# Optimization experiments

Measured on AMD Instinct MI355X. Metric: run time of the kernel, lower is better.

The kernel has to match this reference:

```python
import jax, jax.numpy as jnp
import numpy as np

H = 8          # heads
C = 128        # out_channels per head (hidden_dim)
EMB = 256      # embedding_dim
NG = 64        # number of graphs in batch
EPS_LN = 1e-5


def _layer_norm(x, g, b):
    mu = x.mean(-1, keepdims=True)
    var = ((x - mu) ** 2).mean(-1, keepdims=True)
    return (x - mu) * jax.lax.rsqrt(var + EPS_LN) * g + b


def _transformer_conv(x, src, dst, Wq, bq, Wk, bk, Wv, bv, Ws, bs, Wb):
    # PyG TransformerConv, heads=H, concat=False, beta=True, root_weight=True
    N = x.shape[0]
    q = (x @ Wq + bq).reshape(N, H, C)
    k = (x @ Wk + bk).reshape(N, H, C)
    v = (x @ Wv + bv).reshape(N, H, C)
    # per-edge attention logits: q_i . k_j / sqrt(C)   (i=dst, j=src)
    logits = jnp.einsum('ehc,ehc->eh', q[dst], k[src]) / jnp.sqrt(jnp.asarray(C, x.dtype))
    # segment softmax over incoming edges of each dst node
    m = jax.ops.segment_max(logits, dst, num_segments=N)
    m = jnp.where(jnp.isfinite(m), m, 0.0)
    ex = jnp.exp(logits - m[dst])
    den = jax.ops.segment_sum(ex, dst, num_segments=N)
    alpha = ex / (den[dst] + 1e-16)                      # [E,H]
    msg = alpha[:, :, None] * v[src]                     # [E,H,C]
    out = jax.ops.segment_sum(msg, dst, num_segments=N)  # [N,H,C]
    out = out.mean(axis=1)                               # concat=False -> head mean
    # beta-gated skip connection
    x_r = x @ Ws + bs                                    # [N,C]
    beta = jax.nn.sigmoid(jnp.concatenate([out, x_r, out - x_r], axis=-1) @ Wb)  # [N,1]
    return beta * x_r + (1.0 - beta) * out


def _lin(k, fan_in, fan_out, scale=None):
    s = scale if scale is not None else 1.0 / np.sqrt(fan_in)
    k1, k2 = jax.random.split(k)
    W = jax.random.uniform(k1, (fan_in, fan_out), jnp.float32, -s, s)
    b = jax.random.uniform(k2, (fan_out,), jnp.float32, -s, s)
    return W, b


def setup_inputs() -> dict:
    key = jax.random.key(0)
    ks = jax.random.split(key, 32)
    N, E, V = 50000, 400000, 10000
    inp = {
        'x': jax.random.randint(ks[0], (N,), 0, V, jnp.int32),
        'edge_index': jax.random.randint(ks[1], (2, E), 0, N, jnp.int32),
        'batch': jnp.sort(jax.random.randint(ks[2], (N,), 0, NG, jnp.int32)),
        'emb_w': jax.random.normal(ks[3], (V, EMB), jnp.float32),
    }
    ki = 4
    for l, din in enumerate([EMB, C]):
        Wq, bq = _lin(ks[ki], din, H * C); ki += 1
        Wk, bk = _lin(ks[ki], din, H * C); ki += 1
        Wv, bv = _lin(ks[ki], din, H * C); ki += 1
        Ws, bs = _lin(ks[ki], din, C); ki += 1
        Wb, _ = _lin(ks[ki], 3 * C, 1); ki += 1
        inp.update({f'Wq{l}': Wq, f'bq{l}': bq, f'Wk{l}': Wk, f'bk{l}': bk,
                    f'Wv{l}': Wv, f'bv{l}': bv, f'Ws{l}': Ws, f'bs{l}': bs,
                    f'Wb{l}': Wb, f'g{l}': jnp.ones((C,), jnp.float32),
                    f'be{l}': jnp.zeros((C,), jnp.float32)})
    Wc1, bc1 = _lin(ks[ki], C, C // 2); ki += 1
    Wc2, bc2 = _lin(ks[ki], C // 2, 1); ki += 1
    inp.update({'Wc1': Wc1, 'bc1': bc1, 'Wc2': Wc2, 'bc2': bc2})
    return inp


def reference(x, edge_index, batch, emb_w,
              Wq0, bq0, Wk0, bk0, Wv0, bv0, Ws0, bs0, Wb0, g0, be0,
              Wq1, bq1, Wk1, bk1, Wv1, bv1, Ws1, bs1, Wb1, g1, be1,
              Wc1, bc1, Wc2, bc2):
    src, dst = edge_index[0], edge_index[1]
    h = emb_w[x]                                           # [N, EMB]
    # layer 0 (no residual, per original `if i > 0`)
    h = _transformer_conv(h, src, dst, Wq0, bq0, Wk0, bk0, Wv0, bv0, Ws0, bs0, Wb0)
    h = jax.nn.relu(_layer_norm(h, g0, be0))               # dropout = identity (eval)
    # layer 1 (residual)
    res = h
    h = _transformer_conv(h, src, dst, Wq1, bq1, Wk1, bk1, Wv1, bv1, Ws1, bs1, Wb1)
    h = jax.nn.relu(_layer_norm(h + res, g1, be1))
    # global mean pool over graphs
    s = jax.ops.segment_sum(h, batch, num_segments=NG)     # [NG, C]
    cnt = jax.ops.segment_sum(jnp.ones((h.shape[0],), h.dtype), batch, num_segments=NG)
    pooled = s / jnp.maximum(cnt, 1.0)[:, None]
    # classifier MLP
    z = jax.nn.relu(pooled @ Wc1 + bc1)
    return z @ Wc2 + bc2                                   # [NG, 1]
```

## Files before the change

kernel.cpp:

```cpp
#include <hip/hip_runtime.h>
#include <hip/hip_fp16.h>
#include <math.h>

#define HEADS 8
#define CDIM 128
#define HC 1024
#define EMBD 256
#define NGRAPH 64
#define QSCALE2 0.12751744f

typedef unsigned short u16;
typedef short s8v __attribute__((ext_vector_type(8)));
typedef float f4v __attribute__((ext_vector_type(4)));
typedef _Float16 h2v __attribute__((ext_vector_type(2)));

__device__ __forceinline__ float b2f(u16 u) {
  union { unsigned int i; float f; } v; v.i = ((unsigned int)u) << 16; return v.f;
}
__device__ __forceinline__ u16 f2b(float f) {
  union { float f; unsigned int i; } v; v.f = f;
  unsigned int i = v.i;
  unsigned int r = (i + 0x7FFFu + ((i >> 16) & 1u)) >> 16;
  return (u16)r;
}
__device__ __forceinline__ u16 f2h(float f) {
  __half h = __float2half(f);
  return *(u16*)&h;
}

union U4H { uint4 u; h2v h[4]; };

__global__ __launch_bounds__(256) void embed_kernel(
    const int* __restrict__ x, const float* __restrict__ emb,
    u16* __restrict__ h0, int N)
{
  int idx = blockIdx.x * 256 + threadIdx.x;
  if (idx >= N * (EMBD / 4)) return;
  int n = idx >> 6;
  int j = (idx & 63) * 4;
  int vid = x[n];
  float4 f = *(const float4*)&emb[(size_t)vid * EMBD + j];
  ushort4 u;
  u.x = f2b(f.x); u.y = f2b(f.y); u.z = f2b(f.z); u.w = f2b(f.w);
  *(ushort4*)&h0[(size_t)n * EMBD + j] = u;
}

__global__ __launch_bounds__(256) void build_WsT_swz(
    const float* __restrict__ in, u16* __restrict__ out, int K)
{
  const int KS = K / 32;
  int nt = blockIdx.x;
  int ks = blockIdx.y;
  int t = threadIdx.x;
  int lane = t & 63, ni = t >> 6;
  int q4 = lane >> 4, cn = lane & 15;
  int colL = nt * 64 + ni * 16 + cn;
  int kbase = ks * 32 + q4 * 8;
  u16 tmp[8];
#pragma unroll
  for (int e8 = 0; e8 < 8; e8++) tmp[e8] = f2b(in[(size_t)(kbase + e8) * CDIM + colL]);
  size_t base = ((((size_t)nt * KS + ks) * 4 + ni) * 64 + lane) * 8;
  *(uint4*)&out[base] = *(uint4*)tmp;
}

__global__ __launch_bounds__(256) void build_qkvT_swz(
    const float* __restrict__ Wq, const float* __restrict__ Wk, const float* __restrict__ Wv,
    u16* __restrict__ WT, int K, int hpc)
{
  __shared__ u16 tile[64][130];
  const int KS = K / 32;
  int rg0 = blockIdx.x * 128;
  int kk0 = blockIdx.y * 64;
  int chunkCols = hpc * 384;
  int chunk = rg0 / chunkCols;
  int within = rg0 - chunk * chunkCols;
  int head = chunk * hpc + within / 384;
  int sub = within % 384;
  int sect = sub >> 7;
  const float* W = (sect == 0) ? Wq : (sect == 1 ? Wk : Wv);
  float scale = (sect == 0) ? QSCALE2 : 1.0f;
  int cc0 = head * CDIM;
  int t = threadIdx.x;
  int ci = t & 127, k2 = t >> 7;
#pragma unroll
  for (int ii = 0; ii < 32; ii++) {
    int ki = k2 + ii * 2;
    tile[ki][ci] = f2b(W[(size_t)(kk0 + ki) * HC + cc0 + ci] * scale);
  }
  __syncthreads();

  int lane = t & 63, ni = t >> 6;
  int q4 = lane >> 4, cn = lane & 15;
  int ntBase = rg0 >> 6;
#pragma unroll
  for (int ntd = 0; ntd < 2; ntd++) {
#pragma unroll
    for (int ksd = 0; ksd < 2; ksd++) {
      int colL = ntd * 64 + ni * 16 + cn;
      int kL = ksd * 32 + q4 * 8;
      u16 tmp[8];
#pragma unroll
      for (int e8 = 0; e8 < 8; e8++) tmp[e8] = tile[kL + e8][colL];
      size_t base = ((((size_t)(ntBase + ntd) * KS + (kk0 >> 5) + ksd) * 4 + ni) * 64 + lane) * 8;
      *(uint4*)&WT[base] = *(uint4*)tmp;
    }
  }
}
__global__ __launch_bounds__(256) void build_qkvb(
    const float* __restrict__ bq, const float* __restrict__ bk, const float* __restrict__ bv,
    float* __restrict__ bT, int hpc)
{
  int rg = blockIdx.x * 256 + threadIdx.x;
  if (rg >= 3 * HC) return;
  int chunkCols = hpc * 384;
  int chunk = rg / chunkCols;
  int within = rg - chunk * chunkCols;
  int head = chunk * hpc + within / 384;
  int sub = within % 384;
  int sect = sub >> 7;
  int cc = head * CDIM + (sub & 127);
  bT[rg] = (sect == 0) ? bq[cc] * QSCALE2 : (sect == 1 ? bk[cc] : bv[cc]);
}

__global__ __launch_bounds__(256) void deg_kernel(const int* __restrict__ ei, int* __restrict__ deg, int E) {
  int e = blockIdx.x * 256 + threadIdx.x;
  if (e < E) atomicAdd(&deg[ei[E + e]], 1);
}
__global__ __launch_bounds__(256) void scan1_kernel(const int* __restrict__ deg, int* __restrict__ row_ptr,
                                                    int* __restrict__ bsum, int N) {
  __shared__ int sb[256];
  int t = threadIdx.x, idx = blockIdx.x * 256 + t;
  int x = (idx < N) ? deg[idx] : 0;
  sb[t] = x; __syncthreads();
  for (int off = 1; off < 256; off <<= 1) {
    int y = (t >= off) ? sb[t - off] : 0;
    __syncthreads(); sb[t] += y; __syncthreads();
  }
  if (idx < N) row_ptr[idx + 1] = sb[t];
  if (t == 255) bsum[blockIdx.x] = sb[255];
  if (idx == 0) row_ptr[0] = 0;
}
__global__ __launch_bounds__(256) void scan2_kernel(int* __restrict__ bsum, int B) {
  __shared__ int sb[256];
  int t = threadIdx.x;
  int x = (t < B) ? bsum[t] : 0;
  sb[t] = x; __syncthreads();
  for (int off = 1; off < 256; off <<= 1) {
    int y = (t >= off) ? sb[t - off] : 0;
    __syncthreads(); sb[t] += y; __syncthreads();
  }
  if (t < B) bsum[t] = sb[t] - x;
}
__global__ __launch_bounds__(256) void scan3_kernel(int* __restrict__ row_ptr, const int* __restrict__ bsum, int N) {
  int idx = blockIdx.x * 256 + threadIdx.x;
  if (idx < N) row_ptr[idx + 1] += bsum[idx >> 8];
}
__global__ __launch_bounds__(256) void scatter_kernel(const int* __restrict__ ei,
                                                      const int* __restrict__ row_ptr,
                                                      int* __restrict__ fill, int* __restrict__ col, int E) {
  int e = blockIdx.x * 256 + threadIdx.x;
  if (e >= E) return;
  int d = ei[E + e];
  int pos = row_ptr[d] + atomicAdd(&fill[d], 1);
  col[pos] = ei[e];
}
__global__ void gb_kernel(const int* __restrict__ batch, int* __restrict__ gb, int N) {
  int g = threadIdx.x;
  if (g > NGRAPH) return;
  int lo = 0, hi = N;
  while (lo < hi) { int mid = (lo + hi) >> 1; if (batch[mid] < g) lo = mid + 1; else hi = mid; }
  gb[g] = lo;
}

template <int K>
__global__ __launch_bounds__(256, 3) void gemm_lds(
    const u16* __restrict__ A, const u16* __restrict__ Bq, const u16* __restrict__ Bx,
    int col0tile, int xrTile0,
    const float* __restrict__ biasQ, const float* __restrict__ biasX,
    u16* __restrict__ outQ, u16* __restrict__ outX,
    int M, int nTiles, int rowStrips, int nGroups)
{
  const int LDK = K + 8;
  const int KS = K / 32;
  __shared__ __align__(16) u16 As[64 * LDK];
  int B = blockIdx.x;
  int c8 = B & 7, kk = B >> 3;
  int tg = kk % nGroups;
  int s  = (kk / nGroups) * 8 + c8;
  if (s >= rowStrips) return;
  int t = threadIdx.x, lane = t & 63, w = t >> 6;
  int q4 = lane >> 4, cn = lane & 15;
  int m0 = s * 64;
  int ntL = tg * 4 + w;
  bool wActive = ntL < nTiles;
  int ntG = col0tile + ntL;
  bool isXr = ntG >= xrTile0;

  if (m0 + 64 <= M) {
    const u16* Ablk = A + (size_t)m0 * K;
#pragma unroll
    for (int ii = 0; ii < K / 32; ii++) {
      int g = (ii * 256 + t) * 8;
      int r = g / K, c = g - r * K;
      *(uint4*)&As[r * LDK + c] = *(const uint4*)(Ablk + g);
    }
  } else {
#pragma unroll
    for (int ii = 0; ii < K / 32; ii++) {
      int g = (ii * 256 + t) * 8;
      int r = g / K, c = g - r * K;
      int gr = m0 + r; if (gr >= M) gr = M - 1;
      *(uint4*)&As[r * LDK + c] = *(const uint4*)(A + (size_t)gr * K + c);
    }
  }
  __syncthreads();

  if (!wActive) return;

  f4v acc[4][4] = {};
  const u16* bb = isXr
      ? Bx + ((size_t)(ntG - xrTile0) * KS * 4) * 512 + lane * 8
      : Bq + ((size_t)ntG * KS * 4) * 512 + lane * 8;
#pragma unroll
  for (int ks = 0; ks < KS; ks++) {
    s8v bf[4], af[4];
#pragma unroll
    for (int ni = 0; ni < 4; ni++)
      bf[ni] = *(const s8v*)(bb + ((size_t)ks * 4 + ni) * 512);
#pragma unroll
    for (int mi = 0; mi < 4; mi++)
      af[mi] = *(const s8v*)&As[(mi * 16 + cn) * LDK + ks * 32 + q4 * 8];
#pragma unroll
    for (int mi = 0; mi < 4; mi++)
#pragma unroll
      for (int ni = 0; ni < 4; ni++)
        acc[mi][ni] = __builtin_amdgcn_mfma_f32_16x16x32_bf16(af[mi], bf[ni], acc[mi][ni], 0, 0, 0);
  }

  u16* obase = isXr ? outX + (size_t)(ntG - xrTile0) * M * 64
                    : outQ + (size_t)ntL * M * 64;
  float bv[4];
#pragma unroll
  for (int ni = 0; ni < 4; ni++)
    bv[ni] = isXr ? biasX[(ntG - xrTile0) * 64 + ni * 16 + cn]
                  : biasQ[ntG * 64 + ni * 16 + cn];
#pragma unroll
  for (int mi = 0; mi < 4; mi++) {
#pragma unroll
    for (int j = 0; j < 4; j++) {
      int gm = m0 + mi * 16 + q4 * 4 + j;
      if (gm < M) {
#pragma unroll
        for (int ni = 0; ni < 4; ni++) {
          float val = acc[mi][ni][j] + bv[ni];
          obase[(size_t)gm * 64 + ni * 16 + cn] = isXr ? f2b(val) : f2h(val);
        }
      }
    }
  }
}

template <int HPC>
__global__ __launch_bounds__(256) void attn_chunk_kernel(
    const u16* __restrict__ qkv,
    const int* __restrict__ row_ptr, const int* __restrict__ col,
    float* __restrict__ outacc, int N, int first)
{
  int t = threadIdx.x;
  int w = t >> 6, lane = t & 63;
  int g = lane >> 4, i = lane & 15;
  int n, j;
  if (HPC == 4)      { n = blockIdx.x;                 j = w; }
  else if (HPC == 2) { n = blockIdx.x * 2 + (w >> 1);  j = w & 1; }
  else               { n = blockIdx.x * 4 + w;         j = 0; }
  bool active = (HPC == 4) ? true : (n < N);

  int itile = i >> 3, ioff = (i & 7) * 8;
  const u16* qb = qkv + (size_t)(j * 6 + 0 + itile) * N * 64 + ioff;
  const u16* kb = qkv + (size_t)(j * 6 + 2 + itile) * N * 64 + ioff;
  const u16* vb = qkv + (size_t)(j * 6 + 4 + itile) * N * 64 + ioff;

  float acc[8] = {};
  float m = -INFINITY, l = 0.f;
  if (active) {
    U4H qu; qu.u = *(const uint4*)(qb + (size_t)n * 64);
    int e0 = row_ptr[n], e1 = row_ptr[n + 1];
    for (int eb = e0; eb < e1; eb += 8) {
      int egA = eb + g, egB = eb + 4 + g;
      bool vA = egA < e1, vB = egB < e1;
      int sA = col[vA ? egA : e1 - 1];
      int sB = col[vB ? egB : e1 - 1];
      U4H kuA, vuA, kuB, vuB;
      kuA.u = *(const uint4*)(kb + (size_t)sA * 64);
      kuB.u = *(const uint4*)(kb + (size_t)sB * 64);
      vuA.u = *(const uint4*)(vb + (size_t)sA * 64);
      vuB.u = *(const uint4*)(vb + (size_t)sB * 64);

      float pA, pB;
#if defined(__has_builtin) && __has_builtin(__builtin_amdgcn_fdot2)
      pA = __builtin_amdgcn_fdot2(kuA.h[0], qu.h[0], 0.f, false);
      pA = __builtin_amdgcn_fdot2(kuA.h[1], qu.h[1], pA, false);
      pA = __builtin_amdgcn_fdot2(kuA.h[2], qu.h[2], pA, false);
      pA = __builtin_amdgcn_fdot2(kuA.h[3], qu.h[3], pA, false);
      pB = __builtin_amdgcn_fdot2(kuB.h[0], qu.h[0], 0.f, false);
      pB = __builtin_amdgcn_fdot2(kuB.h[1], qu.h[1], pB, false);
      pB = __builtin_amdgcn_fdot2(kuB.h[2], qu.h[2], pB, false);
      pB = __builtin_amdgcn_fdot2(kuB.h[3], qu.h[3], pB, false);
#else
      pA = 0.f; pB = 0.f;
#pragma unroll
      for (int z = 0; z < 4; z++) {
        pA += (float)kuA.h[z][0] * (float)qu.h[z][0] + (float)kuA.h[z][1] * (float)qu.h[z][1];
        pB += (float)kuB.h[z][0] * (float)qu.h[z][0] + (float)kuB.h[z][1] * (float)qu.h[z][1];
      }
#endif
#pragma unroll
      for (int off = 1; off <= 8; off <<= 1) {
        pA += __shfl_xor(pA, off, 64);
        pB += __shfl_xor(pB, off, 64);
      }
      if (!vA) pA = -INFINITY;
      if (!vB) pB = -INFINITY;

      float pm = fmaxf(pA, pB);
      pm = fmaxf(pm, __shfl_xor(pm, 16));
      pm = fmaxf(pm, __shfl_xor(pm, 32));
      if (pm > m) {
        float al = exp2f(m - pm);
        l *= al;
#pragma unroll
        for (int z = 0; z < 8; z++) acc[z] *= al;
        m = pm;
      }
      float peA = exp2f(pA - m);
      float peB = exp2f(pB - m);
      float ps = peA + peB;
      ps += __shfl_xor(ps, 16);
      ps += __shfl_xor(ps, 32);
      l += ps;
#pragma unroll
      for (int z = 0; z < 4; z++) {
        acc[2 * z]     = fmaf(peA, (float)vuA.h[z][0], acc[2 * z]);
        acc[2 * z + 1] = fmaf(peA, (float)vuA.h[z][1], acc[2 * z + 1]);
      }
#pragma unroll
      for (int z = 0; z < 4; z++) {
        acc[2 * z]     = fmaf(peB, (float)vuB.h[z][0], acc[2 * z]);
        acc[2 * z + 1] = fmaf(peB, (float)vuB.h[z][1], acc[2 * z + 1]);
      }
    }
  }
  float inv = 0.125f / (l + 1e-16f);
#pragma unroll
  for (int z = 0; z < 8; z++) {
    float a = acc[z] * inv;
    a += __shfl_xor(a, 16);
    a += __shfl_xor(a, 32);
    acc[z] = a;
  }

  if (HPC == 1) {
    if (active && g == 0) {
      float* op = outacc + (size_t)n * CDIM + i * 8;
      if (first) {
        *(float4*)op       = make_float4(acc[0], acc[1], acc[2], acc[3]);
        *(float4*)(op + 4) = make_float4(acc[4], acc[5], acc[6], acc[7]);
      } else {
        float4 o0 = *(float4*)op, o1 = *(float4*)(op + 4);
        *(float4*)op       = make_float4(o0.x + acc[0], o0.y + acc[1], o0.z + acc[2], o0.w + acc[3]);
        *(float4*)(op + 4) = make_float4(o1.x + acc[4], o1.y + acc[5], o1.z + acc[6], o1.w + acc[7]);
      }
    }
  } else {
    __shared__ float sacc[4][128];
    if (g == 0) {
      *(float4*)&sacc[w][i * 8]     = make_float4(acc[0], acc[1], acc[2], acc[3]);
      *(float4*)&sacc[w][i * 8 + 4] = make_float4(acc[4], acc[5], acc[6], acc[7]);
    }
    __syncthreads();
    if (HPC == 4) {
      if (t < 128) {
        float v = sacc[0][t] + sacc[1][t] + sacc[2][t] + sacc[3][t];
        size_t o = (size_t)blockIdx.x * CDIM + t;
        outacc[o] = first ? v : (outacc[o] + v);
      }
    } else {
      int nn = blockIdx.x * 2 + (t >> 7);
      int c = t & 127;
      if (nn < N) {
        float v = sacc[(t >> 7) * 2][c] + sacc[(t >> 7) * 2 + 1][c];
        size_t o = (size_t)nn * CDIM + c;
        outacc[o] = first ? v : (outacc[o] + v);
      }
    }
  }
}

template <int LAYER>
__global__ __launch_bounds__(256) void epilogue_kernel(
    const float* __restrict__ outacc, const u16* __restrict__ xrT,
    const float* __restrict__ Wb, const float* __restrict__ gam, const float* __restrict__ bet,
    const u16* __restrict__ res,
    u16* __restrict__ hout, float* __restrict__ houtf, int N)
{
  int t = threadIdx.x;
  int local = t >> 7, c = t & 127, w = t >> 6;
  int n = blockIdx.x * 2 + local;
  bool act = n < N;
  __shared__ float sred[8];
  __shared__ float smv[2][3];

  float oc = 0.f, xc = 0.f;
  if (act) {
    oc = outacc[(size_t)n * CDIM + c];
    xc = b2f(xrT[((size_t)(c >> 6) * N + n) * 64 + (c & 63)]);
  }
  float pb = oc * Wb[c] + xc * Wb[CDIM + c] + (oc - xc) * Wb[2 * CDIM + c];
#pragma unroll
  for (int off = 32; off; off >>= 1) pb += __shfl_down(pb, off, 64);
  if ((t & 63) == 0) sred[w] = pb;
  __syncthreads();
  if (t == 0)   smv[0][0] = 1.f / (1.f + __expf(-(sred[0] + sred[1])));
  if (t == 128) smv[1][0] = 1.f / (1.f + __expf(-(sred[2] + sred[3])));
  __syncthreads();
  float beta = smv[local][0];
  float val = beta * xc + (1.f - beta) * oc;
  if (LAYER == 1 && act) val += b2f(res[(size_t)n * CDIM + c]);

  float s1 = val, s2 = val * val;
#pragma unroll
  for (int off = 32; off; off >>= 1) {
    s1 += __shfl_down(s1, off, 64);
    s2 += __shfl_down(s2, off, 64);
  }
  __syncthreads();
  if ((t & 63) == 0) { sred[w * 2] = s1; sred[w * 2 + 1] = s2; }
  __syncthreads();
  if (t == 0) {
    float S1 = sred[0] + sred[2], S2 = sred[1] + sred[3];
    float mu = S1 * (1.f / CDIM);
    float var = fmaxf(S2 * (1.f / CDIM) - mu * mu, 0.f);
    smv[0][1] = mu; smv[0][2] = 1.f / sqrtf(var + 1e-5f);
  }
  if (t == 128) {
    float S1 = sred[4] + sred[6], S2 = sred[5] + sred[7];
    float mu = S1 * (1.f / CDIM);
    float var = fmaxf(S2 * (1.f / CDIM) - mu * mu, 0.f);
    smv[1][1] = mu; smv[1][2] = 1.f / sqrtf(var + 1e-5f);
  }
  __syncthreads();
  if (act) {
    float y = (val - smv[local][1]) * smv[local][2] * gam[c] + bet[c];
    y = fmaxf(y, 0.f);
    if (LAYER == 0) hout[(size_t)n * CDIM + c] = f2b(y);
    else            houtf[(size_t)n * CDIM + c] = y;
  }
}

__global__ __launch_bounds__(256) void classifier_kernel(
    const float* __restrict__ hf, const int* __restrict__ gb,
    const float* __restrict__ Wc1, const float* __restrict__ bc1,
    const float* __restrict__ Wc2, const float* __restrict__ bc2,
    float* __restrict__ out)
{
  int g = blockIdx.x, t = threadIdx.x;
  int half = t >> 7, c = t & 127;
  int s = gb[g], e = gb[g + 1];
  float acc = 0.f;
  for (int n = s + half; n < e; n += 2) acc += hf[(size_t)n * CDIM + c];
  __shared__ float sb[2][128];
  __shared__ float sp[128], sz[64];
  sb[half][c] = acc;
  __syncthreads();
  float cg = fmaxf((float)(e - s), 1.f);
  if (t < 128) sp[t] = (sb[0][t] + sb[1][t]) / cg;
  __syncthreads();
  if (t < 64) {
    float a = bc1[t];
    for (int cc = 0; cc < 128; cc++) a += sp[cc] * Wc1[cc * 64 + t];
    sz[t] = fmaxf(a, 0.f);
  }
  __syncthreads();
  if (t < 64) {
    float pbv = sz[t] * Wc2[t];
    for (int off = 32; off; off >>= 1) pbv += __shfl_down(pbv, off, 64);
    if (t == 0) out[g] = pbv + bc2[0];
  }
}

extern "C" void kernel_launch(void* const* d_in, const int* in_sizes, int n_in,
                              void* d_out, int out_size, void* d_ws, size_t ws_size,
                              hipStream_t stream)
{
  if (n_in != 30) return;

  const int N = in_sizes[0];
  const int E = in_sizes[1] / 2;

  const int* x     = (const int*)d_in[0];
  const int* ei    = (const int*)d_in[1];
  const int* batch = (const int*)d_in[2];
  const float* emb = (const float*)d_in[3];
  const float* Wq0 = (const float*)d_in[4];  const float* bq0 = (const float*)d_in[5];
  const float* Wk0 = (const float*)d_in[6];  const float* bk0 = (const float*)d_in[7];
  const float* Wv0 = (const float*)d_in[8];  const float* bv0 = (const float*)d_in[9];
  const float* Ws0 = (const float*)d_in[10]; const float* bs0 = (const float*)d_in[11];
  const float* Wb0 = (const float*)d_in[12]; const float* g0  = (const float*)d_in[13]; const float* be0 = (const float*)d_in[14];
  const float* Wq1 = (const float*)d_in[15]; const float* bq1 = (const float*)d_in[16];
  const float* Wk1 = (const float*)d_in[17]; const float* bk1 = (const float*)d_in[18];
  const float* Wv1 = (const float*)d_in[19]; const float* bv1 = (const float*)d_in[20];
  const float* Ws1 = (const float*)d_in[21]; const float* bs1 = (const float*)d_in[22];
  const float* Wb1 = (const float*)d_in[23]; const float* g1  = (const float*)d_in[24]; const float* be1 = (const float*)d_in[25];
  const float* Wc1 = (const float*)d_in[26]; const float* bc1 = (const float*)d_in[27];
  const float* Wc2 = (const float*)d_in[28]; const float* bc2 = (const float*)d_in[29];

  auto rnd = [](size_t b) { return (b + 511) & ~(size_t)511; };
  size_t fixedBytes =
      rnd((size_t)N * CDIM * 4) +
      rnd((size_t)N * EMBD * 2) +
      rnd((size_t)N * CDIM * 2) * 2 +
      rnd((size_t)3 * HC * EMBD * 2) +
      rnd((size_t)3 * HC * CDIM * 2) +
      rnd((size_t)3 * HC * 4) * 2 +
      rnd((size_t)CDIM * EMBD * 2) +
      rnd((size_t)CDIM * CDIM * 2) +
      rnd((size_t)N * 4) * 2 +
      rnd((size_t)(N + 1) * 4) +
      rnd((size_t)E * 4) +
      rnd(256 * 4) +
      rnd(65 * 4);
  int hpc = 1;
  if (ws_size >= fixedBytes + rnd((size_t)N * 4 * 384 * 2)) hpc = 4;
  else if (ws_size >= fixedBytes + rnd((size_t)N * 2 * 384 * 2)) hpc = 2;
  const int chunkCols = hpc * 384;
  const int nchunks = HEADS / hpc;
  const int qkvTiles = chunkCols / 64;

  char* ws = (char*)d_ws;
  size_t off = 0;
  auto alloc = [&](size_t bytes) -> void* {
    void* p = ws + off;
    off += (bytes + 511) & ~(size_t)511;
    return p;
  };
  u16*   qkvc  = (u16*)  alloc((size_t)N * chunkCols * 2);
  float* outacc= (float*)alloc((size_t)N * CDIM * 4);
  u16*   h0    = (u16*)  alloc((size_t)N * EMBD * 2);
  u16*   h1    = (u16*)  alloc((size_t)N * CDIM * 2);
  u16*   xrb   = (u16*)  alloc((size_t)N * CDIM * 2);
  u16*   WT0   = (u16*)  alloc((size_t)3 * HC * EMBD * 2);
  u16*   WT1   = (u16*)  alloc((size_t)3 * HC * CDIM * 2);
  float* bT0   = (float*)alloc((size_t)3 * HC * 4);
  float* bT1   = (float*)alloc((size_t)3 * HC * 4);
  u16*   WsT0  = (u16*)  alloc((size_t)CDIM * EMBD * 2);
  u16*   WsT1  = (u16*)  alloc((size_t)CDIM * CDIM * 2);
  int*   deg   = (int*)  alloc((size_t)N * 4);
  int*   fill  = (int*)  alloc((size_t)N * 4);
  int*   rowp  = (int*)  alloc((size_t)(N + 1) * 4);
  int*   colb  = (int*)  alloc((size_t)E * 4);
  int*   bsum  = (int*)  alloc(256 * 4);
  int*   gb    = (int*)  alloc(65 * 4);

  hipMemsetAsync(deg, 0, (size_t)N * 4, stream);
  hipMemsetAsync(fill, 0, (size_t)N * 4, stream);

  embed_kernel<<<(N * 64 + 255) / 256, 256, 0, stream>>>(x, emb, h0, N);
  { dim3 gT(3 * HC / 128, EMBD / 64);
    build_qkvT_swz<<<gT, 256, 0, stream>>>(Wq0, Wk0, Wv0, WT0, EMBD, hpc); }
  { dim3 gT(3 * HC / 128, CDIM / 64);
    build_qkvT_swz<<<gT, 256, 0, stream>>>(Wq1, Wk1, Wv1, WT1, CDIM, hpc); }
  build_qkvb<<<(3 * HC + 255) / 256, 256, 0, stream>>>(bq0, bk0, bv0, bT0, hpc);
  build_qkvb<<<(3 * HC + 255) / 256, 256, 0, stream>>>(bq1, bk1, bv1, bT1, hpc);
  { dim3 gT(2, EMBD / 32);
    build_WsT_swz<<<gT, 256, 0, stream>>>(Ws0, WsT0, EMBD); }
  { dim3 gT(2, CDIM / 32);
    build_WsT_swz<<<gT, 256, 0, stream>>>(Ws1, WsT1, CDIM); }

  int nb = (N + 255) / 256;
  deg_kernel<<<(E + 255) / 256, 256, 0, stream>>>(ei, deg, E);
  scan1_kernel<<<nb, 256, 0, stream>>>(deg, rowp, bsum, N);
  scan2_kernel<<<1, 256, 0, stream>>>(bsum, nb);
  scan3_kernel<<<nb, 256, 0, stream>>>(rowp, bsum, N);
  scatter_kernel<<<(E + 255) / 256, 256, 0, stream>>>(ei, rowp, fill, colb, E);
  gb_kernel<<<1, 128, 0, stream>>>(batch, gb, N);

  int rowStrips = (N + 63) / 64;
  int sGroups = (rowStrips + 7) / 8;
  float* hfinal = (float*)h0;
  int epiBlocks = (N + 1) / 2;

  if (hpc == 4) {
    for (int layer = 0; layer < 2; layer++) {
      const u16* Ain   = (layer == 0) ? h0 : h1;
      const u16* WT    = (layer == 0) ? WT0 : WT1;
      const float* bT  = (layer == 0) ? bT0 : bT1;
      const u16* WsT   = (layer == 0) ? WsT0 : WsT1;
      const float* bs  = (layer == 0) ? bs0 : bs1;
      const float* Wb  = (layer == 0) ? Wb0 : Wb1;
      const float* gam = (layer == 0) ? g0 : g1;
      const float* bet = (layer == 0) ? be0 : be1;
      int K = (layer == 0) ? EMBD : CDIM;

      int nT0 = qkvTiles + 2;
      int nG0 = (nT0 + 3) / 4, nG1 = (qkvTiles + 3) / 4;
      int grid0 = sGroups * nG0 * 8, grid1 = sGroups * nG1 * 8;
      if (K == EMBD)
        gemm_lds<EMBD><<<grid0, 256, 0, stream>>>(Ain, WT, WsT, 0, qkvTiles, bT, bs, qkvc, xrb, N, nT0, rowStrips, nG0);
      else
        gemm_lds<CDIM><<<grid0, 256, 0, stream>>>(Ain, WT, WsT, 0, qkvTiles, bT, bs, qkvc, xrb, N, nT0, rowStrips, nG0);
      attn_chunk_kernel<4><<<N, 256, 0, stream>>>(qkvc, rowp, colb, outacc, N, 1);
      if (K == EMBD)
        gemm_lds<EMBD><<<grid1, 256, 0, stream>>>(Ain, WT, WsT, qkvTiles, 1 << 30, bT, bs, qkvc, xrb, N, qkvTiles, rowStrips, nG1);
      else
        gemm_lds<CDIM><<<grid1, 256, 0, stream>>>(Ain, WT, WsT, qkvTiles, 1 << 30, bT, bs, qkvc, xrb, N, qkvTiles, rowStrips, nG1);
      attn_chunk_kernel<4><<<N, 256, 0, stream>>>(qkvc, rowp, colb, outacc, N, 0);
      if (layer == 0)
        epilogue_kernel<0><<<epiBlocks, 256, 0, stream>>>(outacc, xrb, Wb, gam, bet,
                                                          (const u16*)nullptr, h1, (float*)nullptr, N);
      else
        epilogue_kernel<1><<<epiBlocks, 256, 0, stream>>>(outacc, xrb, Wb, gam, bet,
                                                          h1, (u16*)nullptr, hfinal, N);
    }
  } else {
    int attnBlocks = (hpc == 2) ? (N + 1) / 2 : (N + 3) / 4;
    for (int layer = 0; layer < 2; layer++) {
      const u16* Ain   = (layer == 0) ? h0 : h1;
      const u16* WT    = (layer == 0) ? WT0 : WT1;
      const float* bT  = (layer == 0) ? bT0 : bT1;
      const u16* WsT   = (layer == 0) ? WsT0 : WsT1;
      const float* bs  = (layer == 0) ? bs0 : bs1;
      const float* Wb  = (layer == 0) ? Wb0 : Wb1;
      const float* gam = (layer == 0) ? g0 : g1;
      const float* bet = (layer == 0) ? be0 : be1;
      int K = (layer == 0) ? EMBD : CDIM;

      int gridXR = sGroups * 1 * 8;
      int nG = (qkvTiles + 3) / 4;
      int gridQ = sGroups * nG * 8;
      if (K == EMBD) gemm_lds<EMBD><<<gridXR, 256, 0, stream>>>(Ain, WT, WsT, 0, 0, bT, bs, qkvc, xrb, N, 2, rowStrips, 1);
      else           gemm_lds<CDIM><<<gridXR, 256, 0, stream>>>(Ain, WT, WsT, 0, 0, bT, bs, qkvc, xrb, N, 2, rowStrips, 1);
      for (int c = 0; c < nchunks; c++) {
        int col0tile = c * qkvTiles;
        if (K == EMBD)
          gemm_lds<EMBD><<<gridQ, 256, 0, stream>>>(Ain, WT, WsT, col0tile, 1 << 30, bT, bs, qkvc, xrb, N, qkvTiles, rowStrips, nG);
        else
          gemm_lds<CDIM><<<gridQ, 256, 0, stream>>>(Ain, WT, WsT, col0tile, 1 << 30, bT, bs, qkvc, xrb, N, qkvTiles, rowStrips, nG);
        int first = (c == 0) ? 1 : 0;
        if (hpc == 2)
          attn_chunk_kernel<2><<<attnBlocks, 256, 0, stream>>>(qkvc, rowp, colb, outacc, N, first);
        else
          attn_chunk_kernel<1><<<attnBlocks, 256, 0, stream>>>(qkvc, rowp, colb, outacc, N, first);
      }
      if (layer == 0)
        epilogue_kernel<0><<<epiBlocks, 256, 0, stream>>>(outacc, xrb, Wb, gam, bet,
                                                          (const u16*)nullptr, h1, (float*)nullptr, N);
      else
        epilogue_kernel<1><<<epiBlocks, 256, 0, stream>>>(outacc, xrb, Wb, gam, bet,
                                                          h1, (u16*)nullptr, hfinal, N);
    }
  }

  classifier_kernel<<<NGRAPH, 256, 0, stream>>>(hfinal, gb, Wc1, bc1, Wc2, bc2,
                                                (float*)d_out);
}
```

Before: 1.073 ms.

## Store Q/K/V chunk row-major per node to make gathers contiguous

```diff
diff --git a/kernel.cpp b/kernel.cpp
--- a/kernel.cpp
+++ b/kernel.cpp
@@ -178,7 +178,7 @@
     int col0tile, int xrTile0,
     const float* __restrict__ biasQ, const float* __restrict__ biasX,
     u16* __restrict__ outQ, u16* __restrict__ outX,
-    int M, int nTiles, int rowStrips, int nGroups)
+    int M, int nTiles, int rowStrips, int nGroups, int outStrideQ)
 {
   const int LDK = K + 8;
   const int KS = K / 32;
@@ -237,23 +237,36 @@
         acc[mi][ni] = __builtin_amdgcn_mfma_f32_16x16x32_bf16(af[mi], bf[ni], acc[mi][ni], 0, 0, 0);
   }
 
-  u16* obase = isXr ? outX + (size_t)(ntG - xrTile0) * M * 64
-                    : outQ + (size_t)ntL * M * 64;
   float bv[4];
 #pragma unroll
   for (int ni = 0; ni < 4; ni++)
     bv[ni] = isXr ? biasX[(ntG - xrTile0) * 64 + ni * 16 + cn]
                   : biasQ[ntG * 64 + ni * 16 + cn];
-#pragma unroll
-  for (int mi = 0; mi < 4; mi++) {
-#pragma unroll
-    for (int j = 0; j < 4; j++) {
-      int gm = m0 + mi * 16 + q4 * 4 + j;
-      if (gm < M) {
-#pragma unroll
-        for (int ni = 0; ni < 4; ni++) {
-          float val = acc[mi][ni][j] + bv[ni];
-          obase[(size_t)gm * 64 + ni * 16 + cn] = isXr ? f2b(val) : f2h(val);
+  if (isXr) {
+    u16* obase = outX + (size_t)(ntG - xrTile0) * M * 64;
+#pragma unroll
+    for (int mi = 0; mi < 4; mi++) {
+#pragma unroll
+      for (int j = 0; j < 4; j++) {
+        int gm = m0 + mi * 16 + q4 * 4 + j;
+        if (gm < M) {
+#pragma unroll
+          for (int ni = 0; ni < 4; ni++)
+            obase[(size_t)gm * 64 + ni * 16 + cn] = f2b(acc[mi][ni][j] + bv[ni]);
+        }
+      }
+    }
+  } else {
+    u16* obase = outQ + (size_t)ntL * 64;
+#pragma unroll
+    for (int mi = 0; mi < 4; mi++) {
+#pragma unroll
+      for (int j = 0; j < 4; j++) {
+        int gm = m0 + mi * 16 + q4 * 4 + j;
+        if (gm < M) {
+#pragma unroll
+          for (int ni = 0; ni < 4; ni++)
+            obase[(size_t)gm * outStrideQ + ni * 16 + cn] = f2h(acc[mi][ni][j] + bv[ni]);
         }
       }
     }
@@ -266,6 +279,7 @@
     const int* __restrict__ row_ptr, const int* __restrict__ col,
     float* __restrict__ outacc, int N, int first)
 {
+  const int STRIDE = HPC * 384;
   int t = threadIdx.x;
   int w = t >> 6, lane = t & 63;
   int g = lane >> 4, i = lane & 15;
@@ -275,15 +289,13 @@
   else               { n = blockIdx.x * 4 + w;         j = 0; }
   bool active = (HPC == 4) ? true : (n < N);
 
-  int itile = i >> 3, ioff = (i & 7) * 8;
-  const u16* qb = qkv + (size_t)(j * 6 + 0 + itile) * N * 64 + ioff;
-  const u16* kb = qkv + (size_t)(j * 6 + 2 + itile) * N * 64 + ioff;
-  const u16* vb = qkv + (size_t)(j * 6 + 4 + itile) * N * 64 + ioff;
+  const u16* kb = qkv + j * 384 + 128 + i * 8;
+  const u16* vb = qkv + j * 384 + 256 + i * 8;
 
   float acc[8] = {};
   float m = -INFINITY, l = 0.f;
   if (active) {
-    U4H qu; qu.u = *(const uint4*)(qb + (size_t)n * 64);
+    U4H qu; qu.u = *(const uint4*)(qkv + (size_t)n * STRIDE + j * 384 + i * 8);
     int e0 = row_ptr[n], e1 = row_ptr[n + 1];
     for (int eb = e0; eb < e1; eb += 8) {
       int egA = eb + g, egB = eb + 4 + g;
@@ -291,10 +303,10 @@
       int sA = col[vA ? egA : e1 - 1];
       int sB = col[vB ? egB : e1 - 1];
       U4H kuA, vuA, kuB, vuB;
-      kuA.u = *(const uint4*)(kb + (size_t)sA * 64);
-      kuB.u = *(const uint4*)(kb + (size_t)sB * 64);
-      vuA.u = *(const uint4*)(vb + (size_t)sA * 64);
-      vuB.u = *(const uint4*)(vb + (size_t)sB * 64);
+      kuA.u = *(const uint4*)(kb + (size_t)sA * STRIDE);
+      kuB.u = *(const uint4*)(kb + (size_t)sB * STRIDE);
+      vuA.u = *(const uint4*)(vb + (size_t)sA * STRIDE);
+      vuB.u = *(const uint4*)(vb + (size_t)sB * STRIDE);
 
       float pA, pB;
 #if defined(__has_builtin) && __has_builtin(__builtin_amdgcn_fdot2)
@@ -605,14 +617,14 @@
       int nG0 = (nT0 + 3) / 4, nG1 = (qkvTiles + 3) / 4;
       int grid0 = sGroups * nG0 * 8, grid1 = sGroups * nG1 * 8;
       if (K == EMBD)
-        gemm_lds<EMBD><<<grid0, 256, 0, stream>>>(Ain, WT, WsT, 0, qkvTiles, bT, bs, qkvc, xrb, N, nT0, rowStrips, nG0);
+        gemm_lds<EMBD><<<grid0, 256, 0, stream>>>(Ain, WT, WsT, 0, qkvTiles, bT, bs, qkvc, xrb, N, nT0, rowStrips, nG0, chunkCols);
       else
-        gemm_lds<CDIM><<<grid0, 256, 0, stream>>>(Ain, WT, WsT, 0, qkvTiles, bT, bs, qkvc, xrb, N, nT0, rowStrips, nG0);
+        gemm_lds<CDIM><<<grid0, 256, 0, stream>>>(Ain, WT, WsT, 0, qkvTiles, bT, bs, qkvc, xrb, N, nT0, rowStrips, nG0, chunkCols);
       attn_chunk_kernel<4><<<N, 256, 0, stream>>>(qkvc, rowp, colb, outacc, N, 1);
       if (K == EMBD)
-        gemm_lds<EMBD><<<grid1, 256, 0, stream>>>(Ain, WT, WsT, qkvTiles, 1 << 30, bT, bs, qkvc, xrb, N, qkvTiles, rowStrips, nG1);
+        gemm_lds<EMBD><<<grid1, 256, 0, stream>>>(Ain, WT, WsT, qkvTiles, 1 << 30, bT, bs, qkvc, xrb, N, qkvTiles, rowStrips, nG1, chunkCols);
       else
-        gemm_lds<CDIM><<<grid1, 256, 0, stream>>>(Ain, WT, WsT, qkvTiles, 1 << 30, bT, bs, qkvc, xrb, N, qkvTiles, rowStrips, nG1);
+        gemm_lds<CDIM><<<grid1, 256, 0, stream>>>(Ain, WT, WsT, qkvTiles, 1 << 30, bT, bs, qkvc, xrb, N, qkvTiles, rowStrips, nG1, chunkCols);
       attn_chunk_kernel<4><<<N, 256, 0, stream>>>(qkvc, rowp, colb, outacc, N, 0);
       if (layer == 0)
         epilogue_kernel<0><<<epiBlocks, 256, 0, stream>>>(outacc, xrb, Wb, gam, bet,
@@ -637,14 +649,14 @@
       int gridXR = sGroups * 1 * 8;
       int nG = (qkvTiles + 3) / 4;
       int gridQ = sGroups * nG * 8;
-      if (K == EMBD) gemm_lds<EMBD><<<gridXR, 256, 0, stream>>>(Ain, WT, WsT, 0, 0, bT, bs, qkvc, xrb, N, 2, rowStrips, 1);
-      else           gemm_lds<CDIM><<<gridXR, 256, 0, stream>>>(Ain, WT, WsT, 0, 0, bT, bs, qkvc, xrb, N, 2, rowStrips, 1);
+      if (K == EMBD) gemm_lds<EMBD><<<gridXR, 256, 0, stream>>>(Ain, WT, WsT, 0, 0, bT, bs, qkvc, xrb, N, 2, rowStrips, 1, chunkCols);
+      else           gemm_lds<CDIM><<<gridXR, 256, 0, stream>>>(Ain, WT, WsT, 0, 0, bT, bs, qkvc, xrb, N, 2, rowStrips, 1, chunkCols);
       for (int c = 0; c < nchunks; c++) {
         int col0tile = c * qkvTiles;
         if (K == EMBD)
-          gemm_lds<EMBD><<<gridQ, 256, 0, stream>>>(Ain, WT, WsT, col0tile, 1 << 30, bT, bs, qkvc, xrb, N, qkvTiles, rowStrips, nG);
+          gemm_lds<EMBD><<<gridQ, 256, 0, stream>>>(Ain, WT, WsT, col0tile, 1 << 30, bT, bs, qkvc, xrb, N, qkvTiles, rowStrips, nG, chunkCols);
         else
-          gemm_lds<CDIM><<<gridQ, 256, 0, stream>>>(Ain, WT, WsT, col0tile, 1 << 30, bT, bs, qkvc, xrb, N, qkvTiles, rowStrips, nG);
+          gemm_lds<CDIM><<<gridQ, 256, 0, stream>>>(Ain, WT, WsT, col0tile, 1 << 30, bT, bs, qkvc, xrb, N, qkvTiles, rowStrips, nG, chunkCols);
         int first = (c == 0) ? 1 : 0;
         if (hpc == 2)
           attn_chunk_kernel<2><<<attnBlocks, 256, 0, stream>>>(qkvc, rowp, colb, outacc, N, first);
```

After: 1.064 ms. Within noise of the previous version (-0.8%).
